# Optimization experiments

Measured on AMD Instinct MI355X. Metric: run time of the kernel, lower is better.

## Reference

```python
import jax, jax.numpy as jnp
import numpy as np


def setup_inputs() -> dict:
    key = jax.random.key(0)
    k1, k2 = jax.random.split(key)
    B, S, W, h = 32, 16, 128, 256
    x = jax.random.normal(k1, (B, S, W, h), dtype=jnp.float32)
    target = jax.random.randint(k2, (B, S, W), 0, 16, dtype=jnp.int32)
    return {"x": x, "target": target}


def reference(x, target):
    # Faithful vectorized form of the nested python-loop Arcface forward.
    s = 5.0
    B, S, W, h = x.shape
    # torch: x = x / x.norm()  (global Frobenius norm over the whole tensor)
    xn = x / jnp.linalg.norm(x)
    # combinations(range(S), 2) == upper-triangle (k=1) indices in row-major order
    ii, jj = np.triu_indices(S, k=1)
    P = ii.shape[0]
    x0 = xn[:, ii]  # [B, P, W, h]
    x1 = xn[:, jj]  # [B, P, W, h]
    # per-pair x0 @ x1.T * s  -> [B, P, W, W]; one fused batched GEMM
    scores = jnp.einsum('bpwh,bpvh->bpwv', x0, x1) * s
    # target construction: (t0[:,None] == t1[None,:]).int().argmax(-1)
    t0 = target[:, ii]  # [B, P, W]
    t1 = target[:, jj]  # [B, P, W]
    eq = (t0[..., :, None] == t1[..., None, :]).astype(jnp.int32)  # [B,P,W,W]
    tgt = jnp.argmax(eq, axis=-1)  # first match index (0 if no match), [B,P,W]
    # torch.cat over the B*P list of [W,W] / [W] chunks == reshape
    return scores.reshape(B * P * W, W), tgt.reshape(B * P * W)
```

## Files before the change

kernel.cpp:

```cpp
#include <hip/hip_runtime.h>


typedef __attribute__((ext_vector_type(8))) short short8;
typedef __attribute__((ext_vector_type(4))) float floatx4;

#define BDIM 256
#define LDA 72

static __device__ __forceinline__ unsigned short f2bf(float f) {
    unsigned int u = __builtin_bit_cast(unsigned int, f);
    u += 0x7FFFu + ((u >> 16) & 1u);
    return (unsigned short)(u >> 16);
}

__global__ void sumsq_kernel(const float* __restrict__ x,
                             float* __restrict__ out, int n4) {
    const float4* x4 = reinterpret_cast<const float4*>(x);
    int tid = blockIdx.x * blockDim.x + threadIdx.x;
    int stride = gridDim.x * blockDim.x;
    float s = 0.f;
    for (int idx = tid; idx < n4; idx += stride) {
        float4 v = x4[idx];
        s += v.x * v.x + v.y * v.y + v.z * v.z + v.w * v.w;
    }
    #pragma unroll
    for (int off = 32; off > 0; off >>= 1) s += __shfl_down(s, off, 64);
    __shared__ float ws[4];
    int lane = threadIdx.x & 63, wv = threadIdx.x >> 6;
    if (lane == 0) ws[wv] = s;
    __syncthreads();
    if (threadIdx.x == 0) {
        atomicAdd(out, ws[0] + ws[1] + ws[2] + ws[3]);
    }
}

__global__ __launch_bounds__(BDIM, 2) void pair_gemm_kernel(
    const float* __restrict__ x, const int* __restrict__ target,
    const float* __restrict__ norm2p, float* __restrict__ out_scores,
    float* __restrict__ out_tgt)
{
    __shared__ __align__(16) unsigned short lds_a[128 * LDA];
    __shared__ __align__(16) unsigned short lds_b[128 * LDA];
    __shared__ int tj_s[128];

    const int bp = blockIdx.x;
    const int b  = bp / 120;
    const int p  = bp - b * 120;
    int i = 0, rem = p;
    while (rem >= 15 - i) { rem -= 15 - i; ++i; }
    const int j = i + 1 + rem;

    const float* Ag = x + (size_t)(b * 16 + i) * (128 * 256);
    const float* Bg = x + (size_t)(b * 16 + j) * (128 * 256);

    const int tid  = threadIdx.x;
    const int lane = tid & 63;
    const int wave = tid >> 6;
    const int wm   = (wave >> 1) * 64;
    const int wn   = (wave & 1)  * 64;
    const int r    = lane & 15;
    const int q    = lane >> 4;

    if (tid < 128) tj_s[tid] = target[(size_t)(b * 16 + j) * 128 + tid];

    floatx4 acc[4][4] = {};

    for (int k0 = 0; k0 < 256; k0 += 64) {
        #pragma unroll
        for (int it = 0; it < 8; ++it) {
            int f   = it * BDIM + tid;
            int row = f >> 4;
            int c4  = (f & 15) * 4;
            float4 av = *reinterpret_cast<const float4*>(Ag + (size_t)row * 256 + k0 + c4);
            float4 bv = *reinterpret_cast<const float4*>(Bg + (size_t)row * 256 + k0 + c4);
            uint2 pa, pb;
            pa.x = (unsigned)f2bf(av.x) | ((unsigned)f2bf(av.y) << 16);
            pa.y = (unsigned)f2bf(av.z) | ((unsigned)f2bf(av.w) << 16);
            pb.x = (unsigned)f2bf(bv.x) | ((unsigned)f2bf(bv.y) << 16);
            pb.y = (unsigned)f2bf(bv.z) | ((unsigned)f2bf(bv.w) << 16);
            *reinterpret_cast<uint2*>(&lds_a[row * LDA + c4]) = pa;
            *reinterpret_cast<uint2*>(&lds_b[row * LDA + c4]) = pb;
        }
        __syncthreads();

        #pragma unroll
        for (int ks = 0; ks < 2; ++ks) {
            short8 af[4], bf[4];
            #pragma unroll
            for (int mt = 0; mt < 4; ++mt)
                af[mt] = *reinterpret_cast<const short8*>(
                    &lds_a[(wm + mt * 16 + r) * LDA + ks * 32 + q * 8]);
            #pragma unroll
            for (int nt = 0; nt < 4; ++nt)
                bf[nt] = *reinterpret_cast<const short8*>(
                    &lds_b[(wn + nt * 16 + r) * LDA + ks * 32 + q * 8]);
            #pragma unroll
            for (int mt = 0; mt < 4; ++mt)
                #pragma unroll
                for (int nt = 0; nt < 4; ++nt)
                    acc[mt][nt] = __builtin_amdgcn_mfma_f32_16x16x32_bf16(
                        af[mt], bf[nt], acc[mt][nt], 0, 0, 0);
        }
        __syncthreads();
    }

    const float scale = 5.0f / norm2p[0];
    float* Cb = out_scores + (size_t)bp * (128 * 128);
    #pragma unroll
    for (int mt = 0; mt < 4; ++mt) {
        #pragma unroll
        for (int nt = 0; nt < 4; ++nt) {
            int col  = wn + nt * 16 + r;
            int row0 = wm + mt * 16 + q * 4;
            #pragma unroll
            for (int e = 0; e < 4; ++e)
                Cb[(size_t)(row0 + e) * 128 + col] = acc[mt][nt][e] * scale;
        }
    }

    if (tid < 128) {
        int t0 = target[(size_t)(b * 16 + i) * 128 + tid];
        int found = 0;
        for (int v = 127; v >= 0; --v)
            if (tj_s[v] == t0) found = v;
        out_tgt[(size_t)bp * 128 + tid] = (float)found;
    }
}

extern "C" void kernel_launch(void* const* d_in, const int* in_sizes, int n_in,
                              void* d_out, int out_size, void* d_ws, size_t ws_size,
                              hipStream_t stream) {
    const float* x      = (const float*)d_in[0];
    const int*   target = (const int*)d_in[1];
    float* out        = (float*)d_out;
    float* out_scores = out;
    float* out_tgt    = out + (size_t)32 * 120 * 128 * 128;
    float* norm2      = (float*)d_ws;

    hipMemsetAsync(d_ws, 0, sizeof(float), stream);
    sumsq_kernel<<<1024, BDIM, 0, stream>>>(x, norm2, in_sizes[0] / 4);
    pair_gemm_kernel<<<32 * 120, BDIM, 0, stream>>>(x, target, norm2,
                                                    out_scores, out_tgt);
}
```

Baseline: 419.6 us.

## Pre-convert input to bf16 once and stream tiles via global-to-LDS loads

A fused pre-pass computes the sum of squares and writes a bf16 copy of x into workspace. The pair GEMM then loads bf16 tiles straight into LDS with global_load_lds, using an XOR swizzle in place of padding. It also swaps MFMA operand order so the epilogue can write float4 rows, and raises occupancy to four blocks per SM. This removes the repeated fp32 reads and per-pair conversions of each slice, which were reused 15 times. The cost is an extra 32MB write, and the path depends on the workspace being large enough.

```diff
diff --git a/kernel.cpp b/kernel.cpp
--- a/kernel.cpp
+++ b/kernel.cpp
@@ -5,14 +5,144 @@
 typedef __attribute__((ext_vector_type(4))) float floatx4;
 
 #define BDIM 256
-#define LDA 72
-
-static __device__ __forceinline__ unsigned short f2bf(float f) {
+#define XB_BYTES (32u * 1024u * 1024u)
+
+static __device__ __forceinline__ unsigned int f2bf(float f) {
     unsigned int u = __builtin_bit_cast(unsigned int, f);
     u += 0x7FFFu + ((u >> 16) & 1u);
-    return (unsigned short)(u >> 16);
-}
-
+    return u >> 16;
+}
+
+static __device__ __forceinline__ void gload_lds16(const unsigned short* g,
+                                                   unsigned short* l) {
+    __builtin_amdgcn_global_load_lds(
+        (const __attribute__((address_space(1))) unsigned int*)g,
+        (__attribute__((address_space(3))) unsigned int*)l, 16, 0, 0);
+}
+
+__global__ void convert_sumsq_kernel(const float* __restrict__ x,
+                                     unsigned short* __restrict__ xb,
+                                     float* __restrict__ norm2, int n8) {
+    const float4* x4 = reinterpret_cast<const float4*>(x);
+    uint4* xb4 = reinterpret_cast<uint4*>(xb);
+    int tid = blockIdx.x * blockDim.x + threadIdx.x;
+    int stride = gridDim.x * blockDim.x;
+    float s = 0.f;
+    for (int c = tid; c < n8; c += stride) {
+        float4 a = x4[2 * c], b = x4[2 * c + 1];
+        s += a.x * a.x + a.y * a.y + a.z * a.z + a.w * a.w;
+        s += b.x * b.x + b.y * b.y + b.z * b.z + b.w * b.w;
+        uint4 pk;
+        pk.x = f2bf(a.x) | (f2bf(a.y) << 16);
+        pk.y = f2bf(a.z) | (f2bf(a.w) << 16);
+        pk.z = f2bf(b.x) | (f2bf(b.y) << 16);
+        pk.w = f2bf(b.z) | (f2bf(b.w) << 16);
+        xb4[c] = pk;
+    }
+    #pragma unroll
+    for (int off = 32; off > 0; off >>= 1) s += __shfl_down(s, off, 64);
+    __shared__ float ws[4];
+    int lane = threadIdx.x & 63, wv = threadIdx.x >> 6;
+    if (lane == 0) ws[wv] = s;
+    __syncthreads();
+    if (threadIdx.x == 0) atomicAdd(norm2, ws[0] + ws[1] + ws[2] + ws[3]);
+}
+
+__global__ __launch_bounds__(BDIM, 4) void pair_gemm_bf16_kernel(
+    const unsigned short* __restrict__ xb, const int* __restrict__ target,
+    const float* __restrict__ norm2p, float* __restrict__ out_scores,
+    float* __restrict__ out_tgt)
+{
+    __shared__ __align__(16) unsigned short lds_a[128 * 64];
+    __shared__ __align__(16) unsigned short lds_b[128 * 64];
+    __shared__ int tj_s[128];
+
+    const int bp = blockIdx.x;
+    const int b  = bp / 120;
+    const int p  = bp - b * 120;
+    int i = 0, rem = p;
+    while (rem >= 15 - i) { rem -= 15 - i; ++i; }
+    const int j = i + 1 + rem;
+
+    const unsigned short* Ag = xb + (size_t)(b * 16 + i) * (128 * 256);
+    const unsigned short* Bg = xb + (size_t)(b * 16 + j) * (128 * 256);
+
+    const int tid  = threadIdx.x;
+    const int lane = tid & 63;
+    const int wave = tid >> 6;
+    const int wrow = (wave >> 1) * 64;
+    const int wcol = (wave & 1)  * 64;
+    const int r    = lane & 15;
+    const int q    = lane >> 4;
+
+    if (tid < 128) tj_s[tid] = target[(size_t)(b * 16 + j) * 128 + tid];
+
+    const int slot0 = wave * 64 + lane;
+    floatx4 acc[4][4] = {};
+
+    for (int k0 = 0; k0 < 256; k0 += 64) {
+        #pragma unroll
+        for (int it = 0; it < 4; ++it) {
+            int slot = it * 256 + slot0;
+            int row  = slot >> 3;
+            int c8   = (slot & 7) ^ (row & 7);
+            const unsigned short* ga = Ag + (size_t)row * 256 + k0 + c8 * 8;
+            const unsigned short* gb = Bg + (size_t)row * 256 + k0 + c8 * 8;
+            unsigned short* la = &lds_a[(size_t)(it * 256 + wave * 64) * 8];
+            unsigned short* lb = &lds_b[(size_t)(it * 256 + wave * 64) * 8];
+            gload_lds16(ga, la);
+            gload_lds16(gb, lb);
+        }
+        __syncthreads();
+
+        #pragma unroll
+        for (int ks = 0; ks < 2; ++ks) {
+            const int swz = ((ks * 4 + q) ^ (r & 7)) * 8;
+            short8 af[4], bf[4];
+            #pragma unroll
+            for (int wt = 0; wt < 4; ++wt)
+                af[wt] = *reinterpret_cast<const short8*>(
+                    &lds_a[(wrow + wt * 16 + r) * 64 + swz]);
+            #pragma unroll
+            for (int vt = 0; vt < 4; ++vt)
+                bf[vt] = *reinterpret_cast<const short8*>(
+                    &lds_b[(wcol + vt * 16 + r) * 64 + swz]);
+            #pragma unroll
+            for (int vt = 0; vt < 4; ++vt)
+                #pragma unroll
+                for (int wt = 0; wt < 4; ++wt)
+                    acc[vt][wt] = __builtin_amdgcn_mfma_f32_16x16x32_bf16(
+                        bf[vt], af[wt], acc[vt][wt], 0, 0, 0);
+        }
+        __syncthreads();
+    }
+
+    const float scale = 5.0f / norm2p[0];
+    float* Cb = out_scores + (size_t)bp * (128 * 128);
+    #pragma unroll
+    for (int wt = 0; wt < 4; ++wt) {
+        const int w = wrow + wt * 16 + r;
+        #pragma unroll
+        for (int vt = 0; vt < 4; ++vt) {
+            float4 o;
+            o.x = acc[vt][wt][0] * scale;
+            o.y = acc[vt][wt][1] * scale;
+            o.z = acc[vt][wt][2] * scale;
+            o.w = acc[vt][wt][3] * scale;
+            *reinterpret_cast<float4*>(&Cb[(size_t)w * 128 + wcol + vt * 16 + q * 4]) = o;
+        }
+    }
+
+    if (tid < 128) {
+        int t0 = target[(size_t)(b * 16 + i) * 128 + tid];
+        int found = 0;
+        for (int v = 127; v >= 0; --v)
+            if (tj_s[v] == t0) found = v;
+        out_tgt[(size_t)bp * 128 + tid] = (float)found;
+    }
+}
+
+#define LDA 72
 __global__ void sumsq_kernel(const float* __restrict__ x,
                              float* __restrict__ out, int n4) {
     const float4* x4 = reinterpret_cast<const float4*>(x);
@@ -29,9 +159,7 @@
     int lane = threadIdx.x & 63, wv = threadIdx.x >> 6;
     if (lane == 0) ws[wv] = s;
     __syncthreads();
-    if (threadIdx.x == 0) {
-        atomicAdd(out, ws[0] + ws[1] + ws[2] + ws[3]);
-    }
+    if (threadIdx.x == 0) atomicAdd(out, ws[0] + ws[1] + ws[2] + ws[3]);
 }
 
 __global__ __launch_bounds__(BDIM, 2) void pair_gemm_kernel(
@@ -74,15 +202,14 @@
             float4 av = *reinterpret_cast<const float4*>(Ag + (size_t)row * 256 + k0 + c4);
             float4 bv = *reinterpret_cast<const float4*>(Bg + (size_t)row * 256 + k0 + c4);
             uint2 pa, pb;
-            pa.x = (unsigned)f2bf(av.x) | ((unsigned)f2bf(av.y) << 16);
-            pa.y = (unsigned)f2bf(av.z) | ((unsigned)f2bf(av.w) << 16);
-            pb.x = (unsigned)f2bf(bv.x) | ((unsigned)f2bf(bv.y) << 16);
-            pb.y = (unsigned)f2bf(bv.z) | ((unsigned)f2bf(bv.w) << 16);
+            pa.x = f2bf(av.x) | (f2bf(av.y) << 16);
+            pa.y = f2bf(av.z) | (f2bf(av.w) << 16);
+            pb.x = f2bf(bv.x) | (f2bf(bv.y) << 16);
+            pb.y = f2bf(bv.z) | (f2bf(bv.w) << 16);
             *reinterpret_cast<uint2*>(&lds_a[row * LDA + c4]) = pa;
             *reinterpret_cast<uint2*>(&lds_b[row * LDA + c4]) = pb;
         }
         __syncthreads();
-
         #pragma unroll
         for (int ks = 0; ks < 2; ++ks) {
             short8 af[4], bf[4];
@@ -135,10 +262,20 @@
     float* out        = (float*)d_out;
     float* out_scores = out;
     float* out_tgt    = out + (size_t)32 * 120 * 128 * 128;
-    float* norm2      = (float*)d_ws;
-
-    hipMemsetAsync(d_ws, 0, sizeof(float), stream);
-    sumsq_kernel<<<1024, BDIM, 0, stream>>>(x, norm2, in_sizes[0] / 4);
-    pair_gemm_kernel<<<32 * 120, BDIM, 0, stream>>>(x, target, norm2,
-                                                    out_scores, out_tgt);
-}
+
+    if (ws_size >= XB_BYTES + 64) {
+        unsigned short* xb = (unsigned short*)d_ws;
+        float* norm2 = (float*)((char*)d_ws + XB_BYTES);
+        hipMemsetAsync(norm2, 0, sizeof(float), stream);
+        convert_sumsq_kernel<<<2048, BDIM, 0, stream>>>(x, xb, norm2,
+                                                        in_sizes[0] / 8);
+        pair_gemm_bf16_kernel<<<32 * 120, BDIM, 0, stream>>>(
+            xb, target, norm2, out_scores, out_tgt);
+    } else {
+        float* norm2 = (float*)d_ws;
+        hipMemsetAsync(norm2, 0, sizeof(float), stream);
+        sumsq_kernel<<<1024, BDIM, 0, stream>>>(x, norm2, in_sizes[0] / 4);
+        pair_gemm_kernel<<<32 * 120, BDIM, 0, stream>>>(x, target, norm2,
+                                                        out_scores, out_tgt);
+    }
+}
```

Result: faster. 369.2 us (-12.0%).
